# Optimization experiments

Measured on AMD Instinct MI355X. Metric: run time of the kernel, lower is better.

Reference implementation:

```python
import jax, jax.numpy as jnp
import numpy as np

DIM, DEPTH, DH, CH, SH = 512, 2, 64, 2, 8
B, T, N = 8, 1024, 2048
CI, SI, FF = CH * DH, SH * DH, 4 * DIM


def layer_norm(x, w, b, eps=1e-5):
    m = jnp.mean(x, -1, keepdims=True)
    v = jnp.var(x, -1, keepdims=True)
    return (x - m) * jax.lax.rsqrt(v + eps) * w + b


def rotate_half(x):
    # interleaved pairs: (x0,x1) -> (-x1,x0)
    x1, x2 = x[..., 0::2], x[..., 1::2]
    return jnp.stack((-x2, x1), axis=-1).reshape(x.shape)


def apply_rot(freqs, x):
    return x * jnp.cos(freqs) + rotate_half(x) * jnp.sin(freqs)


def split_heads(x, h):
    b, t, _ = x.shape
    return x.reshape(b, t, h, -1).transpose(0, 2, 1, 3)


def merge_heads(x):
    b, h, t, d = x.shape
    return x.transpose(0, 2, 1, 3).reshape(b, t, h * d)


def rotary_attn(q, k, v, q_pos, k_pos, heads, mask=None):
    # q:(B,Tq,H*Dh), k/v:(B,Tk,H*Dh), pos:(B,T,Dh); rotate_value=False -> v untouched
    qh, kh, vh = split_heads(q, heads), split_heads(k, heads), split_heads(v, heads)
    qh = apply_rot(q_pos[:, None], qh)
    kh = apply_rot(k_pos[:, None], kh)
    scores = jnp.einsum('bhqd,bhkd->bhqk', qh, kh) * (DH ** -0.5)
    if mask is not None:
        scores = jnp.where(mask, scores, jnp.finfo(scores.dtype).min)
    attn = jax.nn.softmax(scores, axis=-1)
    return merge_heads(jnp.einsum('bhqk,bhkd->bhqd', attn, vh))


def _forward(bin_queries, bin_time_emb, encoder_latents, latent_time_emb,
             ca_lnq_w, ca_lnq_b, ca_lnc_w, ca_lnc_b, ca_wq, ca_wkv, ca_wo, ca_bo,
             sa_ln_w, sa_ln_b, sa_wqkv, sa_wo, sa_bo,
             ffn_ln_w, ffn_ln_b, ffn_w1, ffn_b1, ffn_w2, ffn_b2):
    Tq = bin_queries.shape[1]
    mask = jnp.tril(jnp.ones((Tq, Tq), dtype=bool))[None, None]  # (1,1,T,T) causal
    x = bin_queries
    for l in range(DEPTH):
        # 1) rotary cross-attention to history latents
        xn = layer_norm(x, ca_lnq_w[l], ca_lnq_b[l])
        cn = layer_norm(encoder_latents, ca_lnc_w[l], ca_lnc_b[l])
        q = xn @ ca_wq[l]
        k, v = jnp.split(cn @ ca_wkv[l], 2, axis=-1)
        x = x + rotary_attn(q, k, v, bin_time_emb, latent_time_emb, CH) @ ca_wo[l] + ca_bo[l]
        # 2) causal rotary self-attention over bin queries
        xn = layer_norm(x, sa_ln_w[l], sa_ln_b[l])
        q, k, v = jnp.split(xn @ sa_wqkv[l], 3, axis=-1)
        x = x + rotary_attn(q, k, v, bin_time_emb, bin_time_emb, SH, mask) @ sa_wo[l] + sa_bo[l]
        # 3) pre-LN FFN with GEGLU (mult=4), dropout off in eval
        h = layer_norm(x, ffn_ln_w[l], ffn_ln_b[l])
        a, g = jnp.split(h @ ffn_w1[l] + ffn_b1[l], 2, axis=-1)
        x = x + (a * jax.nn.gelu(g, approximate=False)) @ ffn_w2[l] + ffn_b2[l]
    return x


def setup_inputs() -> dict:
    key = jax.random.key(0)
    ks = jax.random.split(key, 12)
    n = lambda i, shape, s: jax.random.normal(ks[i], shape, dtype=jnp.float32) * s
    return {
        'bin_queries': n(0, (B, T, DIM), 1.0),
        'bin_time_emb': n(1, (B, T, DH), 1.0),
        'encoder_latents': n(2, (B, N, DIM), 1.0),
        'latent_time_emb': n(3, (B, N, DH), 1.0),
        'ca_lnq_w': jnp.ones((DEPTH, DIM)), 'ca_lnq_b': jnp.zeros((DEPTH, DIM)),
        'ca_lnc_w': jnp.ones((DEPTH, DIM)), 'ca_lnc_b': jnp.zeros((DEPTH, DIM)),
        'ca_wq': n(4, (DEPTH, DIM, CI), 0.02), 'ca_wkv': n(5, (DEPTH, DIM, 2 * CI), 0.02),
        'ca_wo': n(6, (DEPTH, CI, DIM), 0.02), 'ca_bo': jnp.zeros((DEPTH, DIM)),
        'sa_ln_w': jnp.ones((DEPTH, DIM)), 'sa_ln_b': jnp.zeros((DEPTH, DIM)),
        'sa_wqkv': n(7, (DEPTH, DIM, 3 * SI), 0.02), 'sa_wo': n(8, (DEPTH, SI, DIM), 0.02),
        'sa_bo': jnp.zeros((DEPTH, DIM)),
        'ffn_ln_w': jnp.ones((DEPTH, DIM)), 'ffn_ln_b': jnp.zeros((DEPTH, DIM)),
        'ffn_w1': n(9, (DEPTH, DIM, 2 * FF), 0.02), 'ffn_b1': jnp.zeros((DEPTH, 2 * FF)),
        'ffn_w2': n(10, (DEPTH, FF, DIM), 0.02), 'ffn_b2': jnp.zeros((DEPTH, DIM)),
    }


def reference(bin_queries, bin_time_emb, encoder_latents, latent_time_emb,
              ca_lnq_w, ca_lnq_b, ca_lnc_w, ca_lnc_b, ca_wq, ca_wkv, ca_wo, ca_bo,
              sa_ln_w, sa_ln_b, sa_wqkv, sa_wo, sa_bo,
              ffn_ln_w, ffn_ln_b, ffn_w1, ffn_b1, ffn_w2, ffn_b2):
    return _forward(bin_queries, bin_time_emb, encoder_latents, latent_time_emb,
                    ca_lnq_w, ca_lnq_b, ca_lnc_w, ca_lnc_b, ca_wq, ca_wkv, ca_wo, ca_bo,
                    sa_ln_w, sa_ln_b, sa_wqkv, sa_wo, sa_bo,
                    ffn_ln_w, ffn_ln_b, ffn_w1, ffn_b1, ffn_w2, ffn_b2)
```

## Files before the change

kernel.cpp:

```cpp
#include <hip/hip_runtime.h>
#include <cstdint>
#include <cstddef>

static constexpr int DIMc = 512;
static constexpr int DHc  = 64;
static constexpr int CHc  = 2;
static constexpr int SHc  = 8;
static constexpr int Bc   = 8;
static constexpr int Tc   = 1024;
static constexpr int Nc   = 2048;
static constexpr int CIc  = CHc * DHc;
static constexpr int SIc  = SHc * DHc;
static constexpr int FFc  = 4 * DIMc;
static constexpr int RQ   = Bc * Tc;
static constexpr int RL   = Bc * Nc;

typedef short bf16x8 __attribute__((ext_vector_type(8)));
typedef float f32x4  __attribute__((ext_vector_type(4)));

__device__ __forceinline__ ushort f2bf(float f) {
  uint32_t u = __builtin_bit_cast(uint32_t, f);
  u += 0x7fffu + ((u >> 16) & 1u);
  return (ushort)(u >> 16);
}
__device__ __forceinline__ float bf2f(ushort h) {
  uint32_t u = ((uint32_t)h) << 16;
  return __builtin_bit_cast(float, u);
}

__device__ __forceinline__ void gload_lds16(const ushort* g, ushort* lds) {
  __builtin_amdgcn_global_load_lds(
      (const __attribute__((address_space(1))) void*)g,
      (__attribute__((address_space(3))) void*)lds, 16, 0, 0);
}

__device__ __forceinline__ float gelu_fast(float g) {
  float u = g * (0.7978845608f + 0.0356774081f * g * g);
  float e = __expf(2.f * u);
  float th = 1.f - 2.f * __builtin_amdgcn_rcpf(1.f + e);
  return 0.5f * g * (1.f + th);
}

__global__ __launch_bounds__(256) void ln_rows(const float* __restrict__ X,
    const float* __restrict__ w, const float* __restrict__ b,
    ushort* __restrict__ out, int rows) {
  int gw = (int)((blockIdx.x * 256 + threadIdx.x) >> 6);
  int lane = threadIdx.x & 63;
  if (gw >= rows) return;
  const float* xr = X + (size_t)gw * DIMc;
  float4 v0 = *(const float4*)(xr + lane * 8);
  float4 v1 = *(const float4*)(xr + lane * 8 + 4);
  float xv[8] = {v0.x, v0.y, v0.z, v0.w, v1.x, v1.y, v1.z, v1.w};
  float s = 0.f, ss = 0.f;
#pragma unroll
  for (int i = 0; i < 8; i++) { s += xv[i]; ss += xv[i] * xv[i]; }
#pragma unroll
  for (int off = 32; off; off >>= 1) { s += __shfl_xor(s, off); ss += __shfl_xor(ss, off); }
  float mean = s * (1.f / DIMc);
  float var = ss * (1.f / DIMc) - mean * mean;
  float r = rsqrtf(var + 1e-5f);
  int c = lane * 8;
  ushort o[8] __attribute__((aligned(16)));
#pragma unroll
  for (int i = 0; i < 8; i++) o[i] = f2bf((xv[i] - mean) * r * w[c + i] + b[c + i]);
  *(uint4*)(out + (size_t)gw * DIMc + c) = *(const uint4*)o;
}

__global__ __launch_bounds__(256) void wtrans_all(
    const float* __restrict__ wq, const float* __restrict__ wkv,
    const float* __restrict__ wo, const float* __restrict__ qkv,
    const float* __restrict__ swo, const float* __restrict__ w1,
    const float* __restrict__ w2, ushort* __restrict__ dst, int layer) {
  constexpr int Ks[7]   = {512, 512, 128, 512, 512, 512, 2048};
  constexpr int Ns[7]   = {128, 256, 512, 1536, 512, 4096, 512};
  constexpr int pre[8]  = {0, 64, 192, 256, 1024, 1280, 3328, 4352};
  constexpr int dOff[7] = {0, 65536, 196608, 262144, 1048576, 1310720, 3407872};
  int bid = blockIdx.x;
  int wid = 0;
#pragma unroll
  for (int i = 1; i < 7; i++) wid += (bid >= pre[i]);
  int tileIdx = bid - pre[wid];
  int K = Ks[wid], N = Ns[wid];
  const float* srcs[7] = {wq, wkv, wo, qkv, swo, w1, w2};
  const float* W = srcs[wid] + (size_t)layer * K * N;
  ushort* Wt = dst + dOff[wid];
  int ntx = N / 32;
  int n0 = (tileIdx % ntx) * 32, k0 = (tileIdx / ntx) * 32;
  __shared__ float tile[32][33];
  int tx = threadIdx.x & 31, ty = threadIdx.x >> 5;
#pragma unroll
  for (int i = 0; i < 32; i += 8)
    tile[ty + i][tx] = W[(size_t)(k0 + ty + i) * N + n0 + tx];
  __syncthreads();
  if (wid == 5) {
#pragma unroll
    for (int i = 0; i < 32; i += 8) {
      int nrow = n0 + ty + i;
      int p = nrow & 2047;
      int rowT = ((p >> 4) << 5) + ((nrow < 2048) ? 0 : 16) + (p & 15);
      Wt[(size_t)rowT * K + k0 + tx] = f2bf(tile[tx][ty + i]);
    }
  } else {
#pragma unroll
    for (int i = 0; i < 32; i += 8)
      Wt[(size_t)(n0 + ty + i) * K + k0 + tx] = f2bf(tile[tx][ty + i]);
  }
}

__global__ __launch_bounds__(256) void vtrans(const ushort* __restrict__ src,
    ushort* __restrict__ dst, int NK, int stride, int colOff) {
  __shared__ ushort tile[32][33];
  int b = blockIdx.z;
  int key0 = blockIdx.x * 32, hd0 = blockIdx.y * 32;
  int HD = gridDim.y * 32;
  int tx = threadIdx.x & 31, ty = threadIdx.x >> 5;
#pragma unroll
  for (int i = 0; i < 32; i += 8)
    tile[ty + i][tx] = src[(size_t)(b * NK + key0 + ty + i) * stride + colOff + hd0 + tx];
  __syncthreads();
#pragma unroll
  for (int i = 0; i < 32; i += 8)
    dst[((size_t)b * HD + hd0 + ty + i) * NK + key0 + tx] = tile[tx][ty + i];
}

template<int MODE>
__global__ __launch_bounds__(256) void gemm128(const ushort* __restrict__ A,
    const ushort* __restrict__ Bt, const float* __restrict__ bias,
    const float* __restrict__ resIn, float* __restrict__ resOut,
    ushort* __restrict__ outB, int M, int N, int K) {
  __shared__ __align__(16) ushort As[128 * 64];
  __shared__ __align__(16) ushort Bs[128 * 64];
  int t = threadIdx.x, wv = t >> 6, lane = t & 63;
  int bm = blockIdx.y, bn = blockIdx.x;
  int fr = lane & 15, g = lane >> 4;
  int wr = (wv >> 1) * 64, wc = (wv & 1) * 64;
  int srow = wv * 32 + (lane >> 3);
  int sslot = lane & 7;
  const ushort* Abase = A + (size_t)(bm * 128) * K;
  const ushort* Bbase = Bt + (size_t)(bn * 128) * K;

  f32x4 acc[4][4] = {};
  for (int k0 = 0; k0 < K; k0 += 64) {
#pragma unroll
    for (int j = 0; j < 4; j++) {
      int r = srow + j * 8;
      int kc = sslot ^ (r & 7);
      gload_lds16(Abase + (size_t)r * K + k0 + kc * 8, As + (wv * 256 + j * 64) * 8);
      gload_lds16(Bbase + (size_t)r * K + k0 + kc * 8, Bs + (wv * 256 + j * 64) * 8);
    }
    __syncthreads();
#pragma unroll
    for (int ks = 0; ks < 2; ks++) {
      bf16x8 af[4], bf[4];
#pragma unroll
      for (int mm = 0; mm < 4; mm++) {
        int row = wr + mm * 16 + fr;
        af[mm] = *(const bf16x8*)(As + row * 64 + (((ks * 4 + g) ^ (row & 7)) * 8));
      }
#pragma unroll
      for (int nn = 0; nn < 4; nn++) {
        int row = wc + nn * 16 + fr;
        bf[nn] = *(const bf16x8*)(Bs + row * 64 + (((ks * 4 + g) ^ (row & 7)) * 8));
      }
#pragma unroll
      for (int mm = 0; mm < 4; mm++)
#pragma unroll
        for (int nn = 0; nn < 4; nn++)
          acc[mm][nn] = __builtin_amdgcn_mfma_f32_16x16x32_bf16(af[mm], bf[nn], acc[mm][nn], 0, 0, 0);
    }
    __syncthreads();
  }

  if (MODE == 2) {
    int NH = N >> 1;
#pragma unroll
    for (int mm = 0; mm < 4; mm++)
#pragma unroll
      for (int np = 0; np < 2; np++) {
        int ocol = bn * 64 + (wc >> 1) + np * 16 + fr;
        float ba = bias[ocol];
        float bg = bias[NH + ocol];
#pragma unroll
        for (int i = 0; i < 4; i++) {
          int gr = bm * 128 + wr + mm * 16 + g * 4 + i;
          float a = acc[mm][np * 2][i] + ba;
          float gv = acc[mm][np * 2 + 1][i] + bg;
          outB[(size_t)gr * NH + ocol] = f2bf(a * gelu_fast(gv));
        }
      }
  } else {
#pragma unroll
    for (int mm = 0; mm < 4; mm++)
#pragma unroll
      for (int nn = 0; nn < 4; nn++)
#pragma unroll
        for (int i = 0; i < 4; i++) {
          int gr = bm * 128 + wr + mm * 16 + g * 4 + i;
          int gc = bn * 128 + wc + nn * 16 + fr;
          float val = acc[mm][nn][i] + (bias ? bias[gc] : 0.f);
          if (MODE == 0) outB[(size_t)gr * N + gc] = f2bf(val);
          else resOut[(size_t)gr * N + gc] = resIn[(size_t)gr * N + gc] + val;
        }
  }
}

template<int MODE>
__global__ __launch_bounds__(256) void gemm128x64(const ushort* __restrict__ A,
    const ushort* __restrict__ Bt, const float* __restrict__ bias,
    const float* __restrict__ resIn, float* __restrict__ resOut,
    ushort* __restrict__ outB, int M, int N, int K) {
  __shared__ __align__(16) ushort As[128 * 64];
  __shared__ __align__(16) ushort Bs[64 * 64];
  int t = threadIdx.x, wv = t >> 6, lane = t & 63;
  int bm = blockIdx.y, bn = blockIdx.x;
  int fr = lane & 15, g = lane >> 4;
  int wr = (wv >> 1) * 64, wc = (wv & 1) * 32;
  const ushort* Abase = A + (size_t)(bm * 128) * K;
  const ushort* Bbase = Bt + (size_t)(bn * 64) * K;

  f32x4 acc[4][2] = {};
  for (int k0 = 0; k0 < K; k0 += 64) {
#pragma unroll
    for (int j = 0; j < 4; j++) {
      int c = j * 256 + wv * 64 + lane;
      int r = c >> 3, s = c & 7;
      int kc = s ^ (r & 7);
      gload_lds16(Abase + (size_t)r * K + k0 + kc * 8, As + (j * 256 + wv * 64) * 8);
      if (j < 2)
        gload_lds16(Bbase + (size_t)r * K + k0 + kc * 8, Bs + (j * 256 + wv * 64) * 8);
    }
    __syncthreads();
#pragma unroll
    for (int ks = 0; ks < 2; ks++) {
      bf16x8 af[4], bf[2];
#pragma unroll
      for (int mm = 0; mm < 4; mm++) {
        int row = wr + mm * 16 + fr;
        af[mm] = *(const bf16x8*)(As + row * 64 + (((ks * 4 + g) ^ (row & 7)) * 8));
      }
#pragma unroll
      for (int nn = 0; nn < 2; nn++) {
        int row = wc + nn * 16 + fr;
        bf[nn] = *(const bf16x8*)(Bs + row * 64 + (((ks * 4 + g) ^ (row & 7)) * 8));
      }
#pragma unroll
      for (int mm = 0; mm < 4; mm++)
#pragma unroll
        for (int nn = 0; nn < 2; nn++)
          acc[mm][nn] = __builtin_amdgcn_mfma_f32_16x16x32_bf16(af[mm], bf[nn], acc[mm][nn], 0, 0, 0);
    }
    __syncthreads();
  }

#pragma unroll
  for (int mm = 0; mm < 4; mm++)
#pragma unroll
    for (int nn = 0; nn < 2; nn++)
#pragma unroll
      for (int i = 0; i < 4; i++) {
        int gr = bm * 128 + wr + mm * 16 + g * 4 + i;
        int gc = bn * 64 + wc + nn * 16 + fr;
        float val = acc[mm][nn][i] + (bias ? bias[gc] : 0.f);
        if (MODE == 0) outB[(size_t)gr * N + gc] = f2bf(val);
        else resOut[(size_t)gr * N + gc] = resIn[(size_t)gr * N + gc] + val;
      }
}

template<int MODE>
__global__ __launch_bounds__(256) void gemm64(const ushort* __restrict__ A,
    const ushort* __restrict__ Bt, const float* __restrict__ bias,
    float* __restrict__ resF, ushort* __restrict__ outB,
    int M, int N, int K) {
  __shared__ __align__(16) ushort As[64][40];
  __shared__ __align__(16) ushort Bs[64][40];
  int t = threadIdx.x;
  int bm = blockIdx.y, bn = blockIdx.x;
  int row = t >> 2, kc = (t & 3) << 3;
  const ushort* aG = A + (size_t)(bm * 64 + row) * K + kc;
  const ushort* bG = Bt + (size_t)(bn * 64 + row) * K + kc;
  int wv = t >> 6, lane = t & 63;
  int wr = (wv >> 1) * 32, wc = (wv & 1) * 32;
  int fr = lane & 15, fk = (lane >> 4) << 3;
  f32x4 acc[2][2] = {};
  for (int k0 = 0; k0 < K; k0 += 32) {
    *(uint4*)&As[row][kc] = *(const uint4*)(aG + k0);
    *(uint4*)&Bs[row][kc] = *(const uint4*)(bG + k0);
    __syncthreads();
    bf16x8 a0 = *(const bf16x8*)&As[wr + fr][fk];
    bf16x8 a1 = *(const bf16x8*)&As[wr + 16 + fr][fk];
    bf16x8 b0 = *(const bf16x8*)&Bs[wc + fr][fk];
    bf16x8 b1 = *(const bf16x8*)&Bs[wc + 16 + fr][fk];
    acc[0][0] = __builtin_amdgcn_mfma_f32_16x16x32_bf16(a0, b0, acc[0][0], 0, 0, 0);
    acc[0][1] = __builtin_amdgcn_mfma_f32_16x16x32_bf16(a0, b1, acc[0][1], 0, 0, 0);
    acc[1][0] = __builtin_amdgcn_mfma_f32_16x16x32_bf16(a1, b0, acc[1][0], 0, 0, 0);
    acc[1][1] = __builtin_amdgcn_mfma_f32_16x16x32_bf16(a1, b1, acc[1][1], 0, 0, 0);
    __syncthreads();
  }
  int cr0 = wr + ((lane >> 4) << 2);
  int cc0 = wc + fr;
#pragma unroll
  for (int mm = 0; mm < 2; mm++)
#pragma unroll
    for (int nn = 0; nn < 2; nn++)
#pragma unroll
      for (int i = 0; i < 4; i++) {
        int gr = bm * 64 + cr0 + mm * 16 + i;
        int gc = bn * 64 + cc0 + nn * 16;
        float val = acc[mm][nn][i] + (bias ? bias[gc] : 0.f);
        if (MODE == 0) outB[(size_t)gr * N + gc] = f2bf(val);
        else resF[(size_t)gr * N + gc] = resF[(size_t)gr * N + gc] + val;
      }
}

__global__ __launch_bounds__(256) void rope_apply(ushort* __restrict__ buf,
    const float* __restrict__ fr, int rows, int stride, int colOff, int H, float scale) {
  int idx = blockIdx.x * 256 + threadIdx.x;
  int total = rows * H * 32;
  if (idx >= total) return;
  int p = idx & 31;
  int h = (idx >> 5) % H;
  int r = idx / (32 * H);
  float f0 = fr[(size_t)r * DHc + 2 * p];
  float f1 = fr[(size_t)r * DHc + 2 * p + 1];
  ushort* bp = buf + (size_t)r * stride + colOff + h * DHc + 2 * p;
  float x0 = bf2f(bp[0]), x1 = bf2f(bp[1]);
  float o0 = (x0 * __cosf(f0) - x1 * __sinf(f0)) * scale;
  float o1 = (x1 * __cosf(f1) + x0 * __sinf(f1)) * scale;
  bp[0] = f2bf(o0); bp[1] = f2bf(o1);
}

template<int CAUSAL>
__global__ __launch_bounds__(256) void attn_mfma(
    const ushort* __restrict__ Q, const ushort* __restrict__ K,
    const ushort* __restrict__ Vt, ushort* __restrict__ O,
    int qStride, int kStride, int kOff, int oStride,
    int Tq, int NK, int H) {
  __shared__ __align__(16) ushort Ks[64 * 64];
  __shared__ __align__(16) ushort Vs[64 * 64];
  __shared__ __align__(16) ushort Ps[4][16 * 72];
  int b = blockIdx.z, h = blockIdx.y, qt = blockIdx.x;
  int t = threadIdx.x, wv = t >> 6, lane = t & 63;
  int g = lane >> 4, fr = lane & 15;
  int qw = qt * 64 + wv * 16;
  int HD = H * 64;

  const ushort* qrow = Q + (size_t)(b * Tq + qw + fr) * qStride + h * 64;
  bf16x8 qlo = *(const bf16x8*)(qrow + g * 8);
  bf16x8 qhi = *(const bf16x8*)(qrow + 32 + g * 8);

  f32x4 o_acc[4] = {};
  float m_run[4], l_run[4];
#pragma unroll
  for (int i = 0; i < 4; i++) { m_run[i] = -1e30f; l_run[i] = 0.f; }

  ushort* Pw = &Ps[wv][0];
  int ntiles = CAUSAL ? (qt + 1) : (NK / 64);
  for (int kt = 0; kt < ntiles; kt++) {
    int k0 = kt * 64;
    __syncthreads();
#pragma unroll
    for (int i = 0; i < 2; i++) {
      int id = t + i * 256;
      int r = id >> 3, c = id & 7;
      uint4 kval = *(const uint4*)(K + (size_t)(b * NK + k0 + r) * kStride + kOff + h * 64 + c * 8);
      *(uint4*)(Ks + r * 64 + ((c ^ (r & 7)) * 8)) = kval;
      uint4 vval = *(const uint4*)(Vt + ((size_t)b * HD + h * 64 + r) * NK + k0 + c * 8);
      *(uint4*)(Vs + r * 64 + ((c ^ (r & 7)) * 8)) = vval;
    }
    __syncthreads();

    f32x4 s[4];
#pragma unroll
    for (int nn = 0; nn < 4; nn++) {
      int row = nn * 16 + fr;
      bf16x8 kf0 = *(const bf16x8*)(Ks + row * 64 + ((g ^ (fr & 7)) * 8));
      bf16x8 kf1 = *(const bf16x8*)(Ks + row * 64 + (((4 + g) ^ (fr & 7)) * 8));
      f32x4 z = {};
      z = __builtin_amdgcn_mfma_f32_16x16x32_bf16(qlo, kf0, z, 0, 0, 0);
      z = __builtin_amdgcn_mfma_f32_16x16x32_bf16(qhi, kf1, z, 0, 0, 0);
      s[nn] = z;
    }
    if (CAUSAL && (k0 + 63 > qw)) {
#pragma unroll
      for (int nn = 0; nn < 4; nn++)
#pragma unroll
        for (int i = 0; i < 4; i++)
          if (k0 + nn * 16 + fr > qw + g * 4 + i) s[nn][i] = -1e30f;
    }
#pragma unroll
    for (int i = 0; i < 4; i++) {
      float tm = fmaxf(fmaxf(s[0][i], s[1][i]), fmaxf(s[2][i], s[3][i]));
#pragma unroll
      for (int off = 8; off; off >>= 1) tm = fmaxf(tm, __shfl_xor(tm, off));
      float mnew = fmaxf(m_run[i], tm);
      float corr = __expf(m_run[i] - mnew);
      float ps = 0.f;
#pragma unroll
      for (int nn = 0; nn < 4; nn++) {
        float p = __expf(s[nn][i] - mnew);
        s[nn][i] = p;
        ps += p;
      }
#pragma unroll
      for (int off = 8; off; off >>= 1) ps += __shfl_xor(ps, off);
      l_run[i] = l_run[i] * corr + ps;
      m_run[i] = mnew;
#pragma unroll
      for (int dd = 0; dd < 4; dd++) o_acc[dd][i] *= corr;
    }
#pragma unroll
    for (int nn = 0; nn < 4; nn++)
#pragma unroll
      for (int i = 0; i < 4; i++)
        Pw[(g * 4 + i) * 72 + nn * 16 + fr] = f2bf(s[nn][i]);
    bf16x8 pa0 = *(const bf16x8*)(Pw + fr * 72 + g * 8);
    bf16x8 pa1 = *(const bf16x8*)(Pw + fr * 72 + 32 + g * 8);
#pragma unroll
    for (int dd = 0; dd < 4; dd++) {
      int row = dd * 16 + fr;
      bf16x8 vf0 = *(const bf16x8*)(Vs + row * 64 + ((g ^ (fr & 7)) * 8));
      bf16x8 vf1 = *(const bf16x8*)(Vs + row * 64 + (((4 + g) ^ (fr & 7)) * 8));
      o_acc[dd] = __builtin_amdgcn_mfma_f32_16x16x32_bf16(pa0, vf0, o_acc[dd], 0, 0, 0);
      o_acc[dd] = __builtin_amdgcn_mfma_f32_16x16x32_bf16(pa1, vf1, o_acc[dd], 0, 0, 0);
    }
  }
#pragma unroll
  for (int dd = 0; dd < 4; dd++)
#pragma unroll
    for (int i = 0; i < 4; i++) {
      size_t oidx = (size_t)(b * Tq + qw + g * 4 + i) * oStride + h * 64 + dd * 16 + fr;
      O[oidx] = f2bf(o_acc[dd][i] / l_run[i]);
    }
}

extern "C" void kernel_launch(void* const* d_in, const int* in_sizes, int n_in,
                              void* d_out, int out_size, void* d_ws, size_t ws_size,
                              hipStream_t stream) {
  const float* bin_queries = (const float*)d_in[0];
  const float* bin_time    = (const float*)d_in[1];
  const float* latents     = (const float*)d_in[2];
  const float* lat_time    = (const float*)d_in[3];
  const float* ca_lnq_w = (const float*)d_in[4];
  const float* ca_lnq_b = (const float*)d_in[5];
  const float* ca_lnc_w = (const float*)d_in[6];
  const float* ca_lnc_b = (const float*)d_in[7];
  const float* ca_wq  = (const float*)d_in[8];
  const float* ca_wkv = (const float*)d_in[9];
  const float* ca_wo  = (const float*)d_in[10];
  const float* ca_bo  = (const float*)d_in[11];
  const float* sa_ln_w = (const float*)d_in[12];
  const float* sa_ln_b = (const float*)d_in[13];
  const float* sa_wqkv = (const float*)d_in[14];
  const float* sa_wo   = (const float*)d_in[15];
  const float* sa_bo   = (const float*)d_in[16];
  const float* ffn_ln_w = (const float*)d_in[17];
  const float* ffn_ln_b = (const float*)d_in[18];
  const float* ffn_w1 = (const float*)d_in[19];
  const float* ffn_b1 = (const float*)d_in[20];
  const float* ffn_w2 = (const float*)d_in[21];
  const float* ffn_b2 = (const float*)d_in[22];

  constexpr size_t X_BYTES = (size_t)RQ * DIMc * 4;
  char* ws = (char*)d_ws;
  float* x = (float*)ws;
  char* A0 = ws + X_BYTES;
  ushort* cn     = (ushort*)(A0);
  ushort* ca_xn  = (ushort*)(A0 + 16777216);
  ushort* qbuf   = (ushort*)(A0 + 25165824);
  ushort* kv     = (ushort*)(A0 + 27262976);
  ushort* ca_att = (ushort*)(A0 + 35651584);
  ushort* vt_c   = (ushort*)(A0 + 37748736);
  ushort* sa_xn  = (ushort*)(A0);
  ushort* qkv    = (ushort*)(A0 + 8388608);
  ushort* sa_att = (ushort*)(A0 + 33554432);
  ushort* vt_s   = (ushort*)(A0 + 41943040);
  ushort* hb     = (ushort*)(A0);
  ushort* ag     = (ushort*)(A0 + 8388608);
  char* W0 = A0 + 109051904;
  ushort* wbase = (ushort*)W0;
  ushort* wqT  = wbase;
  ushort* wkvT = wbase + 65536;
  ushort* woT  = wbase + 196608;
  ushort* qkvT = wbase + 262144;
  ushort* swoT = wbase + 1048576;
  ushort* w1T  = wbase + 1310720;
  ushort* w2T  = wbase + 3407872;

  hipMemcpyAsync(x, bin_queries, X_BYTES, hipMemcpyDeviceToDevice, stream);

  for (int l = 0; l < 2; l++) {
    wtrans_all<<<4352, 256, 0, stream>>>(ca_wq, ca_wkv, ca_wo, sa_wqkv, sa_wo,
                                         ffn_w1, ffn_w2, wbase, l);

    ln_rows<<<RQ / 4, 256, 0, stream>>>(x, ca_lnq_w + l * DIMc, ca_lnq_b + l * DIMc, ca_xn, RQ);
    ln_rows<<<RL / 4, 256, 0, stream>>>(latents, ca_lnc_w + l * DIMc, ca_lnc_b + l * DIMc, cn, RL);
    gemm64<0><<<dim3(CIc / 64, RQ / 64), 256, 0, stream>>>(ca_xn, wqT, nullptr, nullptr, qbuf, RQ, CIc, DIMc);
    gemm128x64<0><<<dim3(2 * CIc / 64, RL / 128), 256, 0, stream>>>(cn, wkvT, nullptr,
        nullptr, nullptr, kv, RL, 2 * CIc, DIMc);
    rope_apply<<<(RQ * CHc * 32) / 256, 256, 0, stream>>>(qbuf, bin_time, RQ, CIc, 0, CHc, 0.125f);
    rope_apply<<<(RL * CHc * 32) / 256, 256, 0, stream>>>(kv, lat_time, RL, 2 * CIc, 0, CHc, 1.f);
    vtrans<<<dim3(Nc / 32, CHc * 64 / 32, Bc), 256, 0, stream>>>(kv, vt_c, Nc, 2 * CIc, CIc);
    attn_mfma<0><<<dim3(Tc / 64, CHc, Bc), 256, 0, stream>>>(qbuf, kv, vt_c, ca_att,
        CIc, 2 * CIc, 0, CIc, Tc, Nc, CHc);
    gemm128x64<1><<<dim3(DIMc / 64, RQ / 128), 256, 0, stream>>>(ca_att, woT, ca_bo + l * DIMc,
        x, x, nullptr, RQ, DIMc, CIc);

    ln_rows<<<RQ / 4, 256, 0, stream>>>(x, sa_ln_w + l * DIMc, sa_ln_b + l * DIMc, sa_xn, RQ);
    gemm128<0><<<dim3(3 * SIc / 128, RQ / 128), 256, 0, stream>>>(sa_xn, qkvT, nullptr,
        nullptr, nullptr, qkv, RQ, 3 * SIc, DIMc);
    rope_apply<<<(RQ * SHc * 32) / 256, 256, 0, stream>>>(qkv, bin_time, RQ, 3 * SIc, 0, SHc, 0.125f);
    rope_apply<<<(RQ * SHc * 32) / 256, 256, 0, stream>>>(qkv, bin_time, RQ, 3 * SIc, SIc, SHc, 1.f);
    vtrans<<<dim3(Tc / 32, SHc * 64 / 32, Bc), 256, 0, stream>>>(qkv, vt_s, Tc, 3 * SIc, 2 * SIc);
    attn_mfma<1><<<dim3(Tc / 64, SHc, Bc), 256, 0, stream>>>(qkv, qkv, vt_s, sa_att,
        3 * SIc, 3 * SIc, SIc, SIc, Tc, Tc, SHc);
    gemm128x64<1><<<dim3(DIMc / 64, RQ / 128), 256, 0, stream>>>(sa_att, swoT, sa_bo + l * DIMc,
        x, x, nullptr, RQ, DIMc, SIc);

    ln_rows<<<RQ / 4, 256, 0, stream>>>(x, ffn_ln_w + l * DIMc, ffn_ln_b + l * DIMc, hb, RQ);
    gemm128<2><<<dim3(2 * FFc / 128, RQ / 128), 256, 0, stream>>>(hb, w1T,
        ffn_b1 + (size_t)l * 2 * FFc, nullptr, nullptr, ag, RQ, 2 * FFc, DIMc);
    float* resOut = (l == 1) ? (float*)d_out : x;
    gemm128x64<1><<<dim3(DIMc / 64, RQ / 128), 256, 0, stream>>>(ag, w2T, ffn_b2 + l * DIMc,
        x, resOut, nullptr, RQ, DIMc, FFc);
  }
}
```

Measured before the change: 734.0 us.

## Transpose attention MFMA operands so each lane owns one query row

The attention kernel swaps the A/B operands of both MFMAs so the score and output accumulators are laid out with the query row per lane and keys/dims along the accumulator index. This collapses the per-row softmax state to one scalar per lane, replaces 4×4 shuffle reductions with two cross-group shuffles, and packs P and output writes into wider 32/64-bit stores. Causal blocks are also launched in reverse order so the longest tiles start first, which should improve load balance. The mask indexing is rewritten to match the new layout, and any mistake there would break correctness.

Measured after the change: 685.7 us. 1.07x faster.

```diff
diff --git a/kernel.cpp b/kernel.cpp
--- a/kernel.cpp
+++ b/kernel.cpp
@@ -22,6 +22,9 @@
   uint32_t u = __builtin_bit_cast(uint32_t, f);
   u += 0x7fffu + ((u >> 16) & 1u);
   return (ushort)(u >> 16);
+}
+__device__ __forceinline__ uint32_t packbf2(float a, float b) {
+  return (uint32_t)f2bf(a) | ((uint32_t)f2bf(b) << 16);
 }
 __device__ __forceinline__ float bf2f(ushort h) {
   uint32_t u = ((uint32_t)h) << 16;
@@ -338,7 +341,8 @@
   __shared__ __align__(16) ushort Ks[64 * 64];
   __shared__ __align__(16) ushort Vs[64 * 64];
   __shared__ __align__(16) ushort Ps[4][16 * 72];
-  int b = blockIdx.z, h = blockIdx.y, qt = blockIdx.x;
+  int b = blockIdx.z, h = blockIdx.y;
+  int qt = CAUSAL ? ((int)gridDim.x - 1 - (int)blockIdx.x) : blockIdx.x;
   int t = threadIdx.x, wv = t >> 6, lane = t & 63;
   int g = lane >> 4, fr = lane & 15;
   int qw = qt * 64 + wv * 16;
@@ -349,11 +353,9 @@
   bf16x8 qhi = *(const bf16x8*)(qrow + 32 + g * 8);
 
   f32x4 o_acc[4] = {};
-  float m_run[4], l_run[4];
-#pragma unroll
-  for (int i = 0; i < 4; i++) { m_run[i] = -1e30f; l_run[i] = 0.f; }
-
-  ushort* Pw = &Ps[wv][0];
+  float m_run = -1e30f, l_run = 0.f;
+
+  uint32_t* Pw = (uint32_t*)&Ps[wv][0];
   int ntiles = CAUSAL ? (qt + 1) : (NK / 64);
   for (int kt = 0; kt < ntiles; kt++) {
     int k0 = kt * 64;
@@ -376,8 +378,8 @@
       bf16x8 kf0 = *(const bf16x8*)(Ks + row * 64 + ((g ^ (fr & 7)) * 8));
       bf16x8 kf1 = *(const bf16x8*)(Ks + row * 64 + (((4 + g) ^ (fr & 7)) * 8));
       f32x4 z = {};
-      z = __builtin_amdgcn_mfma_f32_16x16x32_bf16(qlo, kf0, z, 0, 0, 0);
-      z = __builtin_amdgcn_mfma_f32_16x16x32_bf16(qhi, kf1, z, 0, 0, 0);
+      z = __builtin_amdgcn_mfma_f32_16x16x32_bf16(kf0, qlo, z, 0, 0, 0);
+      z = __builtin_amdgcn_mfma_f32_16x16x32_bf16(kf1, qhi, z, 0, 0, 0);
       s[nn] = z;
     }
     if (CAUSAL && (k0 + 63 > qw)) {
@@ -385,52 +387,57 @@
       for (int nn = 0; nn < 4; nn++)
 #pragma unroll
         for (int i = 0; i < 4; i++)
-          if (k0 + nn * 16 + fr > qw + g * 4 + i) s[nn][i] = -1e30f;
-    }
-#pragma unroll
-    for (int i = 0; i < 4; i++) {
-      float tm = fmaxf(fmaxf(s[0][i], s[1][i]), fmaxf(s[2][i], s[3][i]));
-#pragma unroll
-      for (int off = 8; off; off >>= 1) tm = fmaxf(tm, __shfl_xor(tm, off));
-      float mnew = fmaxf(m_run[i], tm);
-      float corr = __expf(m_run[i] - mnew);
-      float ps = 0.f;
-#pragma unroll
-      for (int nn = 0; nn < 4; nn++) {
+          if (k0 + nn * 16 + g * 4 + i > qw + fr) s[nn][i] = -1e30f;
+    }
+    float tm = s[0][0];
+#pragma unroll
+    for (int nn = 0; nn < 4; nn++)
+#pragma unroll
+      for (int i = 0; i < 4; i++) tm = fmaxf(tm, s[nn][i]);
+    tm = fmaxf(tm, __shfl_xor(tm, 16));
+    tm = fmaxf(tm, __shfl_xor(tm, 32));
+    float mnew = fmaxf(m_run, tm);
+    float corr = __expf(m_run - mnew);
+    float ps = 0.f;
+#pragma unroll
+    for (int nn = 0; nn < 4; nn++)
+#pragma unroll
+      for (int i = 0; i < 4; i++) {
         float p = __expf(s[nn][i] - mnew);
         s[nn][i] = p;
         ps += p;
       }
-#pragma unroll
-      for (int off = 8; off; off >>= 1) ps += __shfl_xor(ps, off);
-      l_run[i] = l_run[i] * corr + ps;
-      m_run[i] = mnew;
-#pragma unroll
-      for (int dd = 0; dd < 4; dd++) o_acc[dd][i] *= corr;
-    }
+    ps += __shfl_xor(ps, 16);
+    ps += __shfl_xor(ps, 32);
+    l_run = l_run * corr + ps;
+    m_run = mnew;
+#pragma unroll
+    for (int dd = 0; dd < 4; dd++) o_acc[dd] *= corr;
 #pragma unroll
     for (int nn = 0; nn < 4; nn++)
 #pragma unroll
-      for (int i = 0; i < 4; i++)
-        Pw[(g * 4 + i) * 72 + nn * 16 + fr] = f2bf(s[nn][i]);
-    bf16x8 pa0 = *(const bf16x8*)(Pw + fr * 72 + g * 8);
-    bf16x8 pa1 = *(const bf16x8*)(Pw + fr * 72 + 32 + g * 8);
+      for (int p = 0; p < 2; p++)
+        Pw[fr * 36 + 8 * nn + 2 * g + p] = packbf2(s[nn][2 * p], s[nn][2 * p + 1]);
+    bf16x8 pa0 = *(const bf16x8*)(&Ps[wv][fr * 72 + g * 8]);
+    bf16x8 pa1 = *(const bf16x8*)(&Ps[wv][fr * 72 + 32 + g * 8]);
 #pragma unroll
     for (int dd = 0; dd < 4; dd++) {
       int row = dd * 16 + fr;
       bf16x8 vf0 = *(const bf16x8*)(Vs + row * 64 + ((g ^ (fr & 7)) * 8));
       bf16x8 vf1 = *(const bf16x8*)(Vs + row * 64 + (((4 + g) ^ (fr & 7)) * 8));
-      o_acc[dd] = __builtin_amdgcn_mfma_f32_16x16x32_bf16(pa0, vf0, o_acc[dd], 0, 0, 0);
-      o_acc[dd] = __builtin_amdgcn_mfma_f32_16x16x32_bf16(pa1, vf1, o_acc[dd], 0, 0, 0);
-    }
-  }
-#pragma unroll
-  for (int dd = 0; dd < 4; dd++)
-#pragma unroll
-    for (int i = 0; i < 4; i++) {
-      size_t oidx = (size_t)(b * Tq + qw + g * 4 + i) * oStride + h * 64 + dd * 16 + fr;
-      O[oidx] = f2bf(o_acc[dd][i] / l_run[i]);
-    }
+      o_acc[dd] = __builtin_amdgcn_mfma_f32_16x16x32_bf16(vf0, pa0, o_acc[dd], 0, 0, 0);
+      o_acc[dd] = __builtin_amdgcn_mfma_f32_16x16x32_bf16(vf1, pa1, o_acc[dd], 0, 0, 0);
+    }
+  }
+  float rl = 1.f / l_run;
+  ushort* obase = O + (size_t)(b * Tq + qw + fr) * oStride + h * 64;
+#pragma unroll
+  for (int dd = 0; dd < 4; dd++) {
+    uint2 w;
+    w.x = packbf2(o_acc[dd][0] * rl, o_acc[dd][1] * rl);
+    w.y = packbf2(o_acc[dd][2] * rl, o_acc[dd][3] * rl);
+    *(uint2*)(obase + dd * 16 + g * 4) = w;
+  }
 }
 
 extern "C" void kernel_launch(void* const* d_in, const int* in_sizes, int n_in,
```
